# Optimization experiments

Measured on AMD Instinct MI355X. Metric: run time of the kernel, lower is better.

## Reference

```python
import jax, jax.numpy as jnp
import numpy as np


def setup_inputs() -> dict:
    key = jax.random.key(0)
    ks = jax.random.split(key, 4)
    B, T, D, H, C = 256, 512, 128, 512, 128
    # xavier-uniform-like scales
    def xavier(k, shape):
        fan_in, fan_out = shape
        lim = np.sqrt(6.0 / (fan_in + fan_out))
        return jax.random.uniform(k, shape, jnp.float32, -lim, lim)
    return {
        "x": jax.random.normal(ks[0], (B, T, D), jnp.float32),
        "Whx": xavier(ks[1], (D, H)),
        "Whh": xavier(ks[2], (H, H)),
        "Wph": xavier(ks[3], (H, C)),
        "bh": jnp.zeros((H,), jnp.float32),
        "bp": jnp.zeros((C,), jnp.float32),
    }


def reference(x, Whx, Whh, Wph, bh, bp):
    B, T, D = x.shape
    H = Whh.shape[0]
    # Precompute input projections for all timesteps in one big GEMM: [B,T,H]
    xproj = jnp.einsum("btd,dh->bth", x, Whx) + bh

    def step(h, xp_t):
        h = jnp.tanh(xp_t + h @ Whh)
        return h, None

    h0 = jnp.zeros((B, H), x.dtype)
    # scan over time: xproj transposed to [T,B,H]
    h_final, _ = jax.lax.scan(step, h0, jnp.swapaxes(xproj, 0, 1))
    return h_final @ Wph + bp
```

## Files before the change

### kernel.cpp

```cpp
#include <hip/hip_runtime.h>
#include <type_traits>

typedef _Float16 f16;
typedef f16 f16x4 __attribute__((ext_vector_type(4)));
typedef f16 f16x8 __attribute__((ext_vector_type(8)));
typedef float f32x4 __attribute__((ext_vector_type(4)));
typedef unsigned int u32;

#define MFMA __builtin_amdgcn_mfma_f32_16x16x32_f16
#define WGSCOPE __HIP_MEMORY_SCOPE_WORKGROUP

constexpr int Bsz = 256, T = 512, D = 128, H = 512, C = 128;
constexpr int ROWS = 16;
constexpr int TPB  = 512;
constexpr int LDH  = H + 8;
constexpr int LDX  = D + 8;
constexpr int NTG  = H / 16;
constexpr int PKT  = 8;
constexpr int KTL  = 3;
constexpr size_t XSTRIDE = (size_t)16 * NTG * 256;

__global__ void pack_w(const float* __restrict__ W, int K, int N, f16* __restrict__ out) {
    int total = K * N;
    int NT = N / 16;
    for (int idx = blockIdx.x * blockDim.x + threadIdx.x; idx < total;
         idx += gridDim.x * blockDim.x) {
        int e    = idx & 7;
        int lane = (idx >> 3) & 63;
        int tile = idx >> 9;
        int kt = tile / NT, nt = tile % NT;
        int k = kt * 32 + 8 * (lane >> 4) + e;
        int n = nt * 16 + (lane & 15);
        out[idx] = (f16)W[(size_t)k * N + n];
    }
}

__device__ __forceinline__ f16x8 load_a(const f16* base, int ld, int kt, int l15, int l4) {
    return *(const f16x8*)(base + l15 * ld + kt * 32 + 8 * l4);
}

__device__ __forceinline__ float fast_tanh(float v) {
    float e = __expf(2.f * v);
    return 1.f - __fdividef(2.f, e + 1.f);
}

template <typename OT>
__global__ __launch_bounds__(TPB, 2) void xproj_k(
    const float* __restrict__ x, const f16* __restrict__ wpack,
    const float* __restrict__ bh, OT* __restrict__ xp) {
    const f16* Whx_p = wpack;
    __shared__ __align__(16) f16 xb[2][ROWS][LDX];
    const int tid = threadIdx.x, lane = tid & 63, w = tid >> 6;
    const int l15 = lane & 15, l4 = lane >> 4;
    const int bt = blockIdx.x;
    const int t0 = blockIdx.y * 16;
    const int b0 = bt * ROWS;
    const int xrow = tid >> 5, xd0 = (tid & 31) * 4;
    const int ntg0 = w * 4;

    float bh4[4];
#pragma unroll
    for (int nt = 0; nt < 4; nt++) bh4[nt] = bh[(ntg0 + nt) * 16 + l15];
    {
        float4 v = *(const float4*)&x[((size_t)(b0 + xrow) * T + t0) * D + xd0];
        f16x4 h4 = {(f16)v.x, (f16)v.y, (f16)v.z, (f16)v.w};
        *(f16x4*)&xb[0][xrow][xd0] = h4;
    }
    __syncthreads();

    int p = 0;
    for (int tt = 0; tt < 16; tt++) {
        int t = t0 + tt;
        float4 xv;
        const bool havex = (tt + 1 < 16);
        if (havex)
            xv = *(const float4*)&x[((size_t)(b0 + xrow) * T + (t + 1)) * D + xd0];
        f32x4 acc[4];
#pragma unroll
        for (int nt = 0; nt < 4; nt++)
            acc[nt] = (f32x4){bh4[nt], bh4[nt], bh4[nt], bh4[nt]};
#pragma unroll
        for (int kt = 0; kt < D / 32; kt++) {
            f16x8 a = load_a(&xb[p][0][0], LDX, kt, l15, l4);
            const f16* btp = Whx_p + (((size_t)kt * NTG + ntg0) * 64 + lane) * 8;
#pragma unroll
            for (int nt = 0; nt < 4; nt++) {
                f16x8 b = *(const f16x8*)(btp + (size_t)nt * 512);
                acc[nt] = MFMA(a, b, acc[nt], 0, 0, 0);
            }
        }
        if (havex) {
            f16x4 h4 = {(f16)xv.x, (f16)xv.y, (f16)xv.z, (f16)xv.w};
            *(f16x4*)&xb[p ^ 1][xrow][xd0] = h4;
        }
        OT* op = xp + (((size_t)t * 16 + bt) * NTG + ntg0) * 256 + (size_t)lane * 4;
#pragma unroll
        for (int nt = 0; nt < 4; nt++) {
            if constexpr (std::is_same_v<OT, float>) {
                *(f32x4*)(op + (size_t)nt * 256) = acc[nt];
            } else {
                f16x4 v = {(f16)acc[nt][0], (f16)acc[nt][1], (f16)acc[nt][2],
                           (f16)acc[nt][3]};
                *(f16x4*)(op + (size_t)nt * 256) = v;
            }
        }
        __syncthreads();
        p ^= 1;
    }
}

template <int XP>
__global__ __launch_bounds__(TPB, 2) void rnn_main(
    const float* __restrict__ x, const f16* __restrict__ wpack,
    const void* __restrict__ xproj, const float* __restrict__ bh,
    const float* __restrict__ bp, float* __restrict__ out) {
    const f16* Whx_p = wpack;
    const f16* Whh_p = wpack + D * H;
    const f16* Wph_p = wpack + D * H + H * H;

    __shared__ __align__(16) f16 hbuf[3][ROWS][LDH];
    __shared__ __align__(16) f16 whh_lds[KTL * NTG * 64 * 8];
    __shared__ u32 pflag[8];
    __shared__ __align__(16) f16 xbuf[(XP == 0) ? 2 : 1][(XP == 0) ? ROWS : 1]
                                     [(XP == 0) ? LDX : 8];

    const int tid = threadIdx.x, lane = tid & 63, w = tid >> 6;
    const int l15 = lane & 15, l4 = lane >> 4;
    const int b0 = blockIdx.x * ROWS;
    const int xrow = tid >> 5, xd0 = (tid & 31) * 4;
    const int ntg0 = w * 4;

    f16x8 wreg[PKT][4];
#pragma unroll
    for (int kt = 0; kt < PKT; kt++)
#pragma unroll
        for (int nt = 0; nt < 4; nt++)
            wreg[kt][nt] =
                *(const f16x8*)(Whh_p + (((size_t)kt * NTG + ntg0 + nt) * 64 + lane) * 8);

    {
        const f16* src = Whh_p + (size_t)PKT * NTG * 512;
        for (int i = tid; i < KTL * NTG * 64; i += TPB)
            *(f16x8*)&whh_lds[(size_t)i * 8] = *(const f16x8*)(src + (size_t)i * 8);
    }
    for (int i = tid; i < ROWS * LDH; i += TPB) (&hbuf[0][0][0])[i] = (f16)0.f;
    if (tid < 8) pflag[tid] = 0u;

    float bh4[4];
    const float* xpf = nullptr;
    const f16* xph = nullptr;
    if constexpr (XP == 1) {
        xpf = (const float*)xproj + (((size_t)blockIdx.x * NTG + ntg0) * 64 + lane) * 4;
    } else if constexpr (XP == 2) {
        xph = (const f16*)xproj + (((size_t)blockIdx.x * NTG + ntg0) * 64 + lane) * 4;
    } else {
#pragma unroll
        for (int nt = 0; nt < 4; nt++) bh4[nt] = bh[(ntg0 + nt) * 16 + l15];
        float4 v = *(const float4*)&x[((size_t)(b0 + xrow) * T + 0) * D + xd0];
        f16x4 h4 = {(f16)v.x, (f16)v.y, (f16)v.z, (f16)v.w};
        *(f16x4*)&xbuf[0][xrow][xd0] = h4;
    }

    f16x8 sA[4], sB[4];
    {
        const f16* wb0 = Whh_p + ((size_t)ntg0 * 64 + lane) * 8;
#pragma unroll
        for (int nt = 0; nt < 4; nt++)
            sA[nt] = *(const f16x8*)(wb0 + ((size_t)11 * NTG + nt) * 512);
#pragma unroll
        for (int nt = 0; nt < 4; nt++)
            sB[nt] = *(const f16x8*)(wb0 + ((size_t)12 * NTG + nt) * 512);
    }
    __syncthreads();
    __builtin_amdgcn_s_setprio(1);

    auto spin = [&](int v, u32 tgt) {
        if constexpr (XP != 0) {
            if (v != w) {
                if (__hip_atomic_load(&pflag[v], __ATOMIC_ACQUIRE, WGSCOPE) >= tgt)
                    return;
                __builtin_amdgcn_s_setprio(0);
                do {
                    __builtin_amdgcn_s_sleep(1);
                } while (__hip_atomic_load(&pflag[v], __ATOMIC_ACQUIRE, WGSCOPE) < tgt);
                __builtin_amdgcn_s_setprio(1);
            }
        }
    };

    auto body = [&](u32 t, const f16* hb, f16* hw, f16x8(&bA)[4], f16x8(&bB)[4],
                    int pp) {
        uintptr_t whu = (uintptr_t)Whh_p;
        asm volatile("" : "+s"(whu));
        const f16* wbase = (const f16*)whu + ((size_t)ntg0 * 64 + lane) * 8;
        u32 zo = 0;
        asm volatile("" : "+v"(zo));
        const f16x8* wlds = (const f16x8*)whh_lds + zo;

        f32x4 xr32[4];
        f16x4 xr16[4];
        if constexpr (XP == 1) {
            const float* xq = xpf + (size_t)t * XSTRIDE;
#pragma unroll
            for (int nt = 0; nt < 4; nt++) xr32[nt] = *(const f32x4*)(xq + (size_t)nt * 256);
        } else if constexpr (XP == 2) {
            const f16* xq = xph + (size_t)t * XSTRIDE;
#pragma unroll
            for (int nt = 0; nt < 4; nt++) xr16[nt] = *(const f16x4*)(xq + (size_t)nt * 256);
        }

        f32x4 acc[4];
        if constexpr (XP == 0) {
#pragma unroll
            for (int nt = 0; nt < 4; nt++)
                acc[nt] = (f32x4){bh4[nt], bh4[nt], bh4[nt], bh4[nt]};
        } else {
#pragma unroll
            for (int nt = 0; nt < 4; nt++) acc[nt] = (f32x4){0.f, 0.f, 0.f, 0.f};
        }

        if constexpr (XP == 0) {
            float4 xv;
            const bool havex = (t + 1 < T);
            if (havex)
                xv = *(const float4*)&x[((size_t)(b0 + xrow) * T + (t + 1)) * D + xd0];
            uintptr_t wxu = (uintptr_t)Whx_p;
            asm volatile("" : "+s"(wxu));
            const f16* wxs = (const f16*)wxu;
#pragma unroll
            for (int kt = 0; kt < D / 32; kt++) {
                f16x8 a = load_a(&xbuf[pp][0][0], LDX, kt, l15, l4);
                const f16* bt = wxs + (((size_t)kt * NTG + ntg0) * 64 + lane) * 8;
#pragma unroll
                for (int nt = 0; nt < 4; nt++) {
                    f16x8 b = *(const f16x8*)(bt + (size_t)nt * 512);
                    acc[nt] = MFMA(a, b, acc[nt], 0, 0, 0);
                }
            }
            if (havex) {
                f16x4 h4 = {(f16)xv.x, (f16)xv.y, (f16)xv.z, (f16)xv.w};
                *(f16x4*)&xbuf[pp ^ 1][xrow][xd0] = h4;
            }
        }

        auto LS = [&](int kt, f16x8(&bf)[4]) {
#pragma unroll
            for (int nt = 0; nt < 4; nt++)
                bf[nt] = *(const f16x8*)(wbase + ((size_t)kt * NTG + nt) * 512);
        };
        auto PK = [&](int kt) {
            f16x8 a = load_a(hb, LDH, kt, l15, l4);
#pragma unroll
            for (int nt = 0; nt < 4; nt++)
                acc[nt] = MFMA(a, wreg[kt][nt], acc[nt], 0, 0, 0);
        };
        auto CL = [&](int ktl) {
            f16x8 a = load_a(hb, LDH, PKT + ktl, l15, l4);
#pragma unroll
            for (int nt = 0; nt < 4; nt++)
                acc[nt] = MFMA(a, wlds[((size_t)ktl * NTG + ntg0 + nt) * 64 + lane],
                               acc[nt], 0, 0, 0);
        };
        auto CS = [&](int kt, f16x8(&bf)[4]) {
            f16x8 a = load_a(hb, LDH, kt, l15, l4);
#pragma unroll
            for (int nt = 0; nt < 4; nt++) acc[nt] = MFMA(a, bf[nt], acc[nt], 0, 0, 0);
        };

        spin(0, t); PK(0); PK(1);
        spin(5, t); CS(11, bA); LS(13, bA);
        spin(1, t); PK(2); PK(3);
        spin(6, t); CS(12, bB); LS(14, bB);
        spin(2, t); PK(4); PK(5);
                    CS(13, bA); LS(15, bA);
        spin(3, t); PK(6); PK(7);
        spin(7, t); CS(14, bB); LS(11, bB);
        spin(4, t); CL(0); CL(1);
                    CS(15, bA); LS(12, bA);
                    CL(2);

#pragma unroll
        for (int nt = 0; nt < 4; nt++)
#pragma unroll
            for (int r = 0; r < 4; r++) {
                float v = acc[nt][r];
                if constexpr (XP == 1) v += xr32[nt][r];
                else if constexpr (XP == 2) v += (float)xr16[nt][r];
                float th = fast_tanh(v);
                hw[(l4 * 4 + r) * LDH + (ntg0 + nt) * 16 + l15] = (f16)th;
            }
        if constexpr (XP != 0) {
            if (lane == 0)
                __hip_atomic_store(&pflag[w], t + 1, __ATOMIC_RELEASE, WGSCOPE);
        } else {
            __syncthreads();
        }
    };

    f16* r0 = &hbuf[0][0][0];
    f16* r1 = &hbuf[1][0][0];
    f16* r2 = &hbuf[2][0][0];
    for (u32 t = 0; t < T; t += 2) {
        body(t,     r0, r1, sA, sB, 0);
        body(t + 1, r1, r2, sB, sA, 1);
        f16* n0 = r2; f16* n1 = r0; f16* n2 = r1;
        r0 = n0; r1 = n1; r2 = n2;
    }

    if constexpr (XP != 0) {
        __builtin_amdgcn_s_setprio(0);
        for (;;) {
            u32 f = __hip_atomic_load(&pflag[lane & 7], __ATOMIC_ACQUIRE, WGSCOPE);
            if (((u32)__ballot(f >= (u32)T) & 0xffu) == 0xffu) break;
            __builtin_amdgcn_s_sleep(1);
        }
        __builtin_amdgcn_s_setprio(1);
    } else {
        __syncthreads();
    }
    {
        float bpv = bp[w * 16 + l15];
        f32x4 acc = {bpv, bpv, bpv, bpv};
#pragma unroll 4
        for (int kt = 0; kt < H / 32; kt++) {
            f16x8 a = load_a(r0, LDH, kt, l15, l4);
            f16x8 b = *(const f16x8*)(Wph_p + (((size_t)kt * (C / 16) + w) * 64 + lane) * 8);
            acc = MFMA(a, b, acc, 0, 0, 0);
        }
#pragma unroll
        for (int r = 0; r < 4; r++)
            out[(size_t)(b0 + l4 * 4 + r) * C + w * 16 + l15] = acc[r];
    }
}

extern "C" void kernel_launch(void* const* d_in, const int* in_sizes, int n_in,
                              void* d_out, int out_size, void* d_ws, size_t ws_size,
                              hipStream_t stream) {
    const float* x   = (const float*)d_in[0];
    const float* Whx = (const float*)d_in[1];
    const float* Whh = (const float*)d_in[2];
    const float* Wph = (const float*)d_in[3];
    const float* bh  = (const float*)d_in[4];
    const float* bp  = (const float*)d_in[5];

    f16* wp = (f16*)d_ws;
    pack_w<<<dim3(128), 256, 0, stream>>>(Whx, D, H, wp);
    pack_w<<<dim3(512), 256, 0, stream>>>(Whh, H, H, wp + D * H);
    pack_w<<<dim3(128), 256, 0, stream>>>(Wph, H, C, wp + D * H + H * H);

    const size_t wbytes = (size_t)(D * H + H * H + H * C) * sizeof(f16);
    const size_t xpel   = (size_t)T * 16 * NTG * 256;

    if (ws_size >= wbytes + xpel * sizeof(float)) {
        float* xpb = (float*)((char*)d_ws + wbytes);
        xproj_k<float><<<dim3(16, T / 16), TPB, 0, stream>>>(x, wp, bh, xpb);
        rnn_main<1><<<dim3(Bsz / ROWS), TPB, 0, stream>>>(x, wp, xpb, bh, bp,
                                                          (float*)d_out);
    } else if (ws_size >= wbytes + xpel * sizeof(f16)) {
        f16* xpb = (f16*)((char*)d_ws + wbytes);
        xproj_k<f16><<<dim3(16, T / 16), TPB, 0, stream>>>(x, wp, bh, xpb);
        rnn_main<2><<<dim3(Bsz / ROWS), TPB, 0, stream>>>(x, wp, xpb, bh, bp,
                                                          (float*)d_out);
    } else {
        rnn_main<0><<<dim3(Bsz / ROWS), TPB, 0, stream>>>(x, wp, nullptr, bh, bp,
                                                          (float*)d_out);
    }
}
```

Measured before the change: 1.439 ms.

## Use four waves per RNN block with more Whh register-resident tiles

The recurrent kernel drops from 8 to 4 waves per block, with each wave owning 8 output tiles instead of 4. Register-resident Whh k-tiles grow from 8 to 13 and the streamed global B-fragment rotation is removed, so each step reads only registers and LDS. The fp32 xproj path is removed and fp16 xproj is always used, halving that traffic at some cost in precision. Risks are register spilling at 104 f16x8 weight registers per lane and fewer waves available to hide MFMA latency.

```diff
diff --git a/kernel.cpp b/kernel.cpp
--- a/kernel.cpp
+++ b/kernel.cpp
@@ -1,5 +1,6 @@
 #include <hip/hip_runtime.h>
 #include <type_traits>
+#include <utility>
 
 typedef _Float16 f16;
 typedef f16 f16x4 __attribute__((ext_vector_type(4)));
@@ -12,11 +13,13 @@
 
 constexpr int Bsz = 256, T = 512, D = 128, H = 512, C = 128;
 constexpr int ROWS = 16;
-constexpr int TPB  = 512;
+constexpr int TPB  = 256;
+constexpr int NW   = 4;
+constexpr int NTW  = 8;
 constexpr int LDH  = H + 8;
 constexpr int LDX  = D + 8;
 constexpr int NTG  = H / 16;
-constexpr int PKT  = 8;
+constexpr int PKT  = 13;
 constexpr int KTL  = 3;
 constexpr size_t XSTRIDE = (size_t)16 * NTG * 256;
 
@@ -44,10 +47,9 @@
     return 1.f - __fdividef(2.f, e + 1.f);
 }
 
-template <typename OT>
-__global__ __launch_bounds__(TPB, 2) void xproj_k(
+__global__ __launch_bounds__(512, 2) void xproj_k(
     const float* __restrict__ x, const f16* __restrict__ wpack,
-    const float* __restrict__ bh, OT* __restrict__ xp) {
+    const float* __restrict__ bh, f16* __restrict__ xp) {
     const f16* Whx_p = wpack;
     __shared__ __align__(16) f16 xb[2][ROWS][LDX];
     const int tid = threadIdx.x, lane = tid & 63, w = tid >> 6;
@@ -93,16 +95,12 @@
             f16x4 h4 = {(f16)xv.x, (f16)xv.y, (f16)xv.z, (f16)xv.w};
             *(f16x4*)&xb[p ^ 1][xrow][xd0] = h4;
         }
-        OT* op = xp + (((size_t)t * 16 + bt) * NTG + ntg0) * 256 + (size_t)lane * 4;
+        f16* op = xp + (((size_t)t * 16 + bt) * NTG + ntg0) * 256 + (size_t)lane * 4;
 #pragma unroll
         for (int nt = 0; nt < 4; nt++) {
-            if constexpr (std::is_same_v<OT, float>) {
-                *(f32x4*)(op + (size_t)nt * 256) = acc[nt];
-            } else {
-                f16x4 v = {(f16)acc[nt][0], (f16)acc[nt][1], (f16)acc[nt][2],
-                           (f16)acc[nt][3]};
-                *(f16x4*)(op + (size_t)nt * 256) = v;
-            }
+            f16x4 v = {(f16)acc[nt][0], (f16)acc[nt][1], (f16)acc[nt][2],
+                       (f16)acc[nt][3]};
+            *(f16x4*)(op + (size_t)nt * 256) = v;
         }
         __syncthreads();
         p ^= 1;
@@ -110,7 +108,7 @@
 }
 
 template <int XP>
-__global__ __launch_bounds__(TPB, 2) void rnn_main(
+__global__ __launch_bounds__(TPB, 1) void rnn_main(
     const float* __restrict__ x, const f16* __restrict__ wpack,
     const void* __restrict__ xproj, const float* __restrict__ bh,
     const float* __restrict__ bp, float* __restrict__ out) {
@@ -120,21 +118,21 @@
 
     __shared__ __align__(16) f16 hbuf[3][ROWS][LDH];
     __shared__ __align__(16) f16 whh_lds[KTL * NTG * 64 * 8];
-    __shared__ u32 pflag[8];
+    __shared__ u32 pflag[NW];
     __shared__ __align__(16) f16 xbuf[(XP == 0) ? 2 : 1][(XP == 0) ? ROWS : 1]
                                      [(XP == 0) ? LDX : 8];
 
     const int tid = threadIdx.x, lane = tid & 63, w = tid >> 6;
     const int l15 = lane & 15, l4 = lane >> 4;
     const int b0 = blockIdx.x * ROWS;
-    const int xrow = tid >> 5, xd0 = (tid & 31) * 4;
-    const int ntg0 = w * 4;
-
-    f16x8 wreg[PKT][4];
+    const int xrow = tid >> 4, xc = (tid & 15) * 8;
+    const int ntg0 = w * NTW;
+
+    f16x8 wreg[PKT][NTW];
 #pragma unroll
     for (int kt = 0; kt < PKT; kt++)
 #pragma unroll
-        for (int nt = 0; nt < 4; nt++)
+        for (int nt = 0; nt < NTW; nt++)
             wreg[kt][nt] =
                 *(const f16x8*)(Whh_p + (((size_t)kt * NTG + ntg0 + nt) * 64 + lane) * 8);
 
@@ -144,86 +142,69 @@
             *(f16x8*)&whh_lds[(size_t)i * 8] = *(const f16x8*)(src + (size_t)i * 8);
     }
     for (int i = tid; i < ROWS * LDH; i += TPB) (&hbuf[0][0][0])[i] = (f16)0.f;
-    if (tid < 8) pflag[tid] = 0u;
-
-    float bh4[4];
-    const float* xpf = nullptr;
+    if (tid < NW) pflag[tid] = 0u;
+
+    float bh8[NTW];
     const f16* xph = nullptr;
-    if constexpr (XP == 1) {
-        xpf = (const float*)xproj + (((size_t)blockIdx.x * NTG + ntg0) * 64 + lane) * 4;
-    } else if constexpr (XP == 2) {
+    if constexpr (XP == 2) {
         xph = (const f16*)xproj + (((size_t)blockIdx.x * NTG + ntg0) * 64 + lane) * 4;
     } else {
 #pragma unroll
-        for (int nt = 0; nt < 4; nt++) bh4[nt] = bh[(ntg0 + nt) * 16 + l15];
-        float4 v = *(const float4*)&x[((size_t)(b0 + xrow) * T + 0) * D + xd0];
-        f16x4 h4 = {(f16)v.x, (f16)v.y, (f16)v.z, (f16)v.w};
-        *(f16x4*)&xbuf[0][xrow][xd0] = h4;
-    }
-
-    f16x8 sA[4], sB[4];
-    {
-        const f16* wb0 = Whh_p + ((size_t)ntg0 * 64 + lane) * 8;
-#pragma unroll
-        for (int nt = 0; nt < 4; nt++)
-            sA[nt] = *(const f16x8*)(wb0 + ((size_t)11 * NTG + nt) * 512);
-#pragma unroll
-        for (int nt = 0; nt < 4; nt++)
-            sB[nt] = *(const f16x8*)(wb0 + ((size_t)12 * NTG + nt) * 512);
+        for (int nt = 0; nt < NTW; nt++) bh8[nt] = bh[(ntg0 + nt) * 16 + l15];
+        const float* xr0 = &x[((size_t)(b0 + xrow) * T + 0) * D + xc];
+        float4 v0 = *(const float4*)xr0;
+        float4 v1 = *(const float4*)(xr0 + 4);
+        f16x4 h0 = {(f16)v0.x, (f16)v0.y, (f16)v0.z, (f16)v0.w};
+        f16x4 h1 = {(f16)v1.x, (f16)v1.y, (f16)v1.z, (f16)v1.w};
+        *(f16x4*)&xbuf[0][xrow][xc] = h0;
+        *(f16x4*)&xbuf[0][xrow][xc + 4] = h1;
     }
     __syncthreads();
     __builtin_amdgcn_s_setprio(1);
 
     auto spin = [&](int v, u32 tgt) {
-        if constexpr (XP != 0) {
-            if (v != w) {
-                if (__hip_atomic_load(&pflag[v], __ATOMIC_ACQUIRE, WGSCOPE) >= tgt)
-                    return;
-                __builtin_amdgcn_s_setprio(0);
-                do {
-                    __builtin_amdgcn_s_sleep(1);
-                } while (__hip_atomic_load(&pflag[v], __ATOMIC_ACQUIRE, WGSCOPE) < tgt);
-                __builtin_amdgcn_s_setprio(1);
-            }
+        if (v != w) {
+            if (__hip_atomic_load(&pflag[v], __ATOMIC_ACQUIRE, WGSCOPE) >= tgt)
+                return;
+            __builtin_amdgcn_s_setprio(0);
+            do {
+                __builtin_amdgcn_s_sleep(1);
+            } while (__hip_atomic_load(&pflag[v], __ATOMIC_ACQUIRE, WGSCOPE) < tgt);
+            __builtin_amdgcn_s_setprio(1);
         }
     };
 
-    auto body = [&](u32 t, const f16* hb, f16* hw, f16x8(&bA)[4], f16x8(&bB)[4],
-                    int pp) {
-        uintptr_t whu = (uintptr_t)Whh_p;
-        asm volatile("" : "+s"(whu));
-        const f16* wbase = (const f16*)whu + ((size_t)ntg0 * 64 + lane) * 8;
+    auto body = [&](u32 t, const f16* hb, f16* hw, int pp) {
         u32 zo = 0;
         asm volatile("" : "+v"(zo));
         const f16x8* wlds = (const f16x8*)whh_lds + zo;
 
-        f32x4 xr32[4];
-        f16x4 xr16[4];
-        if constexpr (XP == 1) {
-            const float* xq = xpf + (size_t)t * XSTRIDE;
-#pragma unroll
-            for (int nt = 0; nt < 4; nt++) xr32[nt] = *(const f32x4*)(xq + (size_t)nt * 256);
-        } else if constexpr (XP == 2) {
+        f16x4 xr16[NTW];
+        if constexpr (XP == 2) {
             const f16* xq = xph + (size_t)t * XSTRIDE;
 #pragma unroll
-            for (int nt = 0; nt < 4; nt++) xr16[nt] = *(const f16x4*)(xq + (size_t)nt * 256);
-        }
-
-        f32x4 acc[4];
+            for (int nt = 0; nt < NTW; nt++)
+                xr16[nt] = *(const f16x4*)(xq + (size_t)nt * 256);
+        }
+
+        f32x4 acc[NTW];
         if constexpr (XP == 0) {
 #pragma unroll
-            for (int nt = 0; nt < 4; nt++)
-                acc[nt] = (f32x4){bh4[nt], bh4[nt], bh4[nt], bh4[nt]};
+            for (int nt = 0; nt < NTW; nt++)
+                acc[nt] = (f32x4){bh8[nt], bh8[nt], bh8[nt], bh8[nt]};
         } else {
 #pragma unroll
-            for (int nt = 0; nt < 4; nt++) acc[nt] = (f32x4){0.f, 0.f, 0.f, 0.f};
+            for (int nt = 0; nt < NTW; nt++) acc[nt] = (f32x4){0.f, 0.f, 0.f, 0.f};
         }
 
         if constexpr (XP == 0) {
-            float4 xv;
+            float4 xv0, xv1;
             const bool havex = (t + 1 < T);
-            if (havex)
-                xv = *(const float4*)&x[((size_t)(b0 + xrow) * T + (t + 1)) * D + xd0];
+            if (havex) {
+                const float* xr = &x[((size_t)(b0 + xrow) * T + (t + 1)) * D + xc];
+                xv0 = *(const float4*)xr;
+                xv1 = *(const float4*)(xr + 4);
+            }
             uintptr_t wxu = (uintptr_t)Whx_p;
             asm volatile("" : "+s"(wxu));
             const f16* wxs = (const f16*)wxu;
@@ -232,60 +213,50 @@
                 f16x8 a = load_a(&xbuf[pp][0][0], LDX, kt, l15, l4);
                 const f16* bt = wxs + (((size_t)kt * NTG + ntg0) * 64 + lane) * 8;
 #pragma unroll
-                for (int nt = 0; nt < 4; nt++) {
+                for (int nt = 0; nt < NTW; nt++) {
                     f16x8 b = *(const f16x8*)(bt + (size_t)nt * 512);
                     acc[nt] = MFMA(a, b, acc[nt], 0, 0, 0);
                 }
             }
             if (havex) {
-                f16x4 h4 = {(f16)xv.x, (f16)xv.y, (f16)xv.z, (f16)xv.w};
-                *(f16x4*)&xbuf[pp ^ 1][xrow][xd0] = h4;
-            }
-        }
-
-        auto LS = [&](int kt, f16x8(&bf)[4]) {
-#pragma unroll
-            for (int nt = 0; nt < 4; nt++)
-                bf[nt] = *(const f16x8*)(wbase + ((size_t)kt * NTG + nt) * 512);
+                f16x4 h0 = {(f16)xv0.x, (f16)xv0.y, (f16)xv0.z, (f16)xv0.w};
+                f16x4 h1 = {(f16)xv1.x, (f16)xv1.y, (f16)xv1.z, (f16)xv1.w};
+                *(f16x4*)&xbuf[pp ^ 1][xrow][xc] = h0;
+                *(f16x4*)&xbuf[pp ^ 1][xrow][xc + 4] = h1;
+            }
+        }
+
+        auto pos = [&](auto ktc) {
+            constexpr int kt = decltype(ktc)::value;
+            if constexpr (XP != 0) {
+                if constexpr ((kt & 3) == 0) spin(kt >> 2, t);
+            }
+            f16x8 a = load_a(hb, LDH, kt, l15, l4);
+            if constexpr (kt < PKT) {
+#pragma unroll
+                for (int nt = 0; nt < NTW; nt++)
+                    acc[nt] = MFMA(a, wreg[kt][nt], acc[nt], 0, 0, 0);
+            } else {
+#pragma unroll
+                for (int nt = 0; nt < NTW; nt++)
+                    acc[nt] = MFMA(
+                        a, wlds[((size_t)(kt - PKT) * NTG + ntg0 + nt) * 64 + lane],
+                        acc[nt], 0, 0, 0);
+            }
         };
-        auto PK = [&](int kt) {
-            f16x8 a = load_a(hb, LDH, kt, l15, l4);
-#pragma unroll
-            for (int nt = 0; nt < 4; nt++)
-                acc[nt] = MFMA(a, wreg[kt][nt], acc[nt], 0, 0, 0);
-        };
-        auto CL = [&](int ktl) {
-            f16x8 a = load_a(hb, LDH, PKT + ktl, l15, l4);
-#pragma unroll
-            for (int nt = 0; nt < 4; nt++)
-                acc[nt] = MFMA(a, wlds[((size_t)ktl * NTG + ntg0 + nt) * 64 + lane],
-                               acc[nt], 0, 0, 0);
-        };
-        auto CS = [&](int kt, f16x8(&bf)[4]) {
-            f16x8 a = load_a(hb, LDH, kt, l15, l4);
-#pragma unroll
-            for (int nt = 0; nt < 4; nt++) acc[nt] = MFMA(a, bf[nt], acc[nt], 0, 0, 0);
-        };
-
-        spin(0, t); PK(0); PK(1);
-        spin(5, t); CS(11, bA); LS(13, bA);
-        spin(1, t); PK(2); PK(3);
-        spin(6, t); CS(12, bB); LS(14, bB);
-        spin(2, t); PK(4); PK(5);
-                    CS(13, bA); LS(15, bA);
-        spin(3, t); PK(6); PK(7);
-        spin(7, t); CS(14, bB); LS(11, bB);
-        spin(4, t); CL(0); CL(1);
-                    CS(15, bA); LS(12, bA);
-                    CL(2);
-
-#pragma unroll
-        for (int nt = 0; nt < 4; nt++)
+#define POS(J) pos(std::integral_constant<int, J>{})
+        POS(0);  POS(1);  POS(2);  POS(3);
+        POS(4);  POS(5);  POS(6);  POS(7);
+        POS(8);  POS(9);  POS(10); POS(11);
+        POS(12); POS(13); POS(14); POS(15);
+#undef POS
+
+#pragma unroll
+        for (int nt = 0; nt < NTW; nt++)
 #pragma unroll
             for (int r = 0; r < 4; r++) {
                 float v = acc[nt][r];
-                if constexpr (XP == 1) v += xr32[nt][r];
-                else if constexpr (XP == 2) v += (float)xr16[nt][r];
+                if constexpr (XP == 2) v += (float)xr16[nt][r];
                 float th = fast_tanh(v);
                 hw[(l4 * 4 + r) * LDH + (ntg0 + nt) * 16 + l15] = (f16)th;
             }
@@ -300,18 +271,20 @@
     f16* r0 = &hbuf[0][0][0];
     f16* r1 = &hbuf[1][0][0];
     f16* r2 = &hbuf[2][0][0];
-    for (u32 t = 0; t < T; t += 2) {
-        body(t,     r0, r1, sA, sB, 0);
-        body(t + 1, r1, r2, sB, sA, 1);
-        f16* n0 = r2; f16* n1 = r0; f16* n2 = r1;
-        r0 = n0; r1 = n1; r2 = n2;
+#pragma unroll 1
+    for (u32 t = 0; t < T; t++) {
+        body(t, r0, r1, (int)(t & 1));
+        f16* tmp = r0;
+        r0 = r1;
+        r1 = r2;
+        r2 = tmp;
     }
 
     if constexpr (XP != 0) {
         __builtin_amdgcn_s_setprio(0);
         for (;;) {
-            u32 f = __hip_atomic_load(&pflag[lane & 7], __ATOMIC_ACQUIRE, WGSCOPE);
-            if (((u32)__ballot(f >= (u32)T) & 0xffu) == 0xffu) break;
+            u32 f = __hip_atomic_load(&pflag[lane & 3], __ATOMIC_ACQUIRE, WGSCOPE);
+            if (((u32)__ballot(f >= (u32)T) & 0xfu) == 0xfu) break;
             __builtin_amdgcn_s_sleep(1);
         }
         __builtin_amdgcn_s_setprio(1);
@@ -319,17 +292,22 @@
         __syncthreads();
     }
     {
-        float bpv = bp[w * 16 + l15];
-        f32x4 acc = {bpv, bpv, bpv, bpv};
+#pragma unroll
+        for (int e = 0; e < 2; e++) {
+            const int ct = w * 2 + e;
+            float bpv = bp[ct * 16 + l15];
+            f32x4 acc = {bpv, bpv, bpv, bpv};
 #pragma unroll 4
-        for (int kt = 0; kt < H / 32; kt++) {
-            f16x8 a = load_a(r0, LDH, kt, l15, l4);
-            f16x8 b = *(const f16x8*)(Wph_p + (((size_t)kt * (C / 16) + w) * 64 + lane) * 8);
-            acc = MFMA(a, b, acc, 0, 0, 0);
-        }
-#pragma unroll
-        for (int r = 0; r < 4; r++)
-            out[(size_t)(b0 + l4 * 4 + r) * C + w * 16 + l15] = acc[r];
+            for (int kt = 0; kt < H / 32; kt++) {
+                f16x8 a = load_a(r0, LDH, kt, l15, l4);
+                f16x8 b =
+                    *(const f16x8*)(Wph_p + (((size_t)kt * (C / 16) + ct) * 64 + lane) * 8);
+                acc = MFMA(a, b, acc, 0, 0, 0);
+            }
+#pragma unroll
+            for (int r = 0; r < 4; r++)
+                out[(size_t)(b0 + l4 * 4 + r) * C + ct * 16 + l15] = acc[r];
+        }
     }
 }
 
@@ -351,14 +329,9 @@
     const size_t wbytes = (size_t)(D * H + H * H + H * C) * sizeof(f16);
     const size_t xpel   = (size_t)T * 16 * NTG * 256;
 
-    if (ws_size >= wbytes + xpel * sizeof(float)) {
-        float* xpb = (float*)((char*)d_ws + wbytes);
-        xproj_k<float><<<dim3(16, T / 16), TPB, 0, stream>>>(x, wp, bh, xpb);
-        rnn_main<1><<<dim3(Bsz / ROWS), TPB, 0, stream>>>(x, wp, xpb, bh, bp,
-                                                          (float*)d_out);
-    } else if (ws_size >= wbytes + xpel * sizeof(f16)) {
+    if (ws_size >= wbytes + xpel * sizeof(f16)) {
         f16* xpb = (f16*)((char*)d_ws + wbytes);
-        xproj_k<f16><<<dim3(16, T / 16), TPB, 0, stream>>>(x, wp, bh, xpb);
+        xproj_k<<<dim3(16, T / 16), 512, 0, stream>>>(x, wp, bh, xpb);
         rnn_main<2><<<dim3(Bsz / ROWS), TPB, 0, stream>>>(x, wp, xpb, bh, bp,
                                                           (float*)d_out);
     } else {
```

Measured after the change: 1.970 ms. 1.37x slower.
